# Kernel optimization log

Hardware: AMD Instinct MI355X
Metric: run time of the kernel (lower is better)

## Reference

```python
import jax, jax.numpy as jnp
import numpy as np
from jax import lax

B, T, C, K = 16, 1024, 512, 5
PAD = (K - 1) // 2
EPS_LN = 1e-5
EPS_BN = 1e-5


def setup_inputs() -> dict:
    key = jax.random.key(0)
    ks = jax.random.split(key, 8)
    s1 = 1.0 / np.sqrt(C)          # fan-in of pointwise conv1 (C -> 2C)
    s2 = 1.0 / np.sqrt(2 * C * K)  # fan-in of k=5 conv (2C -> 2C)
    s3 = 1.0 / np.sqrt(C)          # fan-in of pointwise conv3 (C -> C)
    return {
        "x": jax.random.normal(ks[0], (B, T, C), jnp.float32),
        "ln_g": jnp.ones((C,), jnp.float32),
        "ln_b": jnp.zeros((C,), jnp.float32),
        "w1": (jax.random.normal(ks[1], (2 * C, C), jnp.float32) * s1),
        "b1": jnp.zeros((2 * C,), jnp.float32),
        "w2": (jax.random.normal(ks[2], (K, 2 * C, 2 * C), jnp.float32) * s2),  # WIO layout
        "b2": jnp.zeros((2 * C,), jnp.float32),
        "bn_g": jnp.ones((C,), jnp.float32),
        "bn_b": jnp.zeros((C,), jnp.float32),
        "bn_mean": jax.random.normal(ks[3], (C,), jnp.float32) * 0.1,
        "bn_var": jax.random.uniform(ks[4], (C,), jnp.float32, 0.5, 1.5),
        "w3": (jax.random.normal(ks[5], (C, C), jnp.float32) * s3),
        "b3": jnp.zeros((C,), jnp.float32),
    }


def reference(x, ln_g, ln_b, w1, b1, w2, b2, bn_g, bn_b, bn_mean, bn_var, w3, b3):
    # LayerNorm over channel dim (B, T, C)
    mu = jnp.mean(x, axis=-1, keepdims=True)
    var = jnp.mean(jnp.square(x - mu), axis=-1, keepdims=True)
    h = (x - mu) * lax.rsqrt(var + EPS_LN) * ln_g + ln_b

    # pointwise conv C -> 2C (kernel 1 == GEMM), then Swish
    h = jnp.einsum('btc,oc->bto', h, w1) + b1        # (B, T, 2C)
    h = h * jax.nn.sigmoid(h)

    # kernel-5 conv 2C -> 2C, 'same' padding, channels-last
    h = lax.conv_general_dilated(
        h, w2, window_strides=(1,), padding=[(PAD, PAD)],
        dimension_numbers=('NWC', 'WIO', 'NWC')) + b2  # (B, T, 2C)

    # GLU over channel dim: first half * sigmoid(second half)
    a, g = h[..., :C], h[..., C:]
    h = a * jax.nn.sigmoid(g)                        # (B, T, C)

    # BatchNorm1d(C), eval mode (running stats)
    h = (h - bn_mean) * lax.rsqrt(bn_var + EPS_BN) * bn_g + bn_b

    # pointwise conv C -> C; dropout is identity at inference.
    # Torch output is sequential(...)(B,C,T).transpose(1,2) -> (B, T, C)
    return jnp.einsum('btc,oc->bto', h, w3) + b3
```

## Files before the change

kernel.cpp:

```cpp
#include <hip/hip_runtime.h>
#include <cstdint>


#define NB    16
#define TT    1024
#define CC    512
#define C2    1024
#define TPAD  1028

typedef unsigned short u16;
typedef short bf16x8 __attribute__((ext_vector_type(8)));
typedef float f32x4  __attribute__((ext_vector_type(4)));
typedef __attribute__((address_space(3))) u16 lds_u16;
typedef const __attribute__((address_space(1))) u16 glb_u16;

__device__ __forceinline__ float bf2f(u16 u) {
  union { unsigned int i; float f; } v; v.i = ((unsigned int)u) << 16; return v.f;
}
__device__ __forceinline__ u16 f2bf(float f) {
  union { float f; unsigned int i; } v; v.f = f;
  unsigned int x = v.i;
  return (u16)((x + 0x7fffu + ((x >> 16) & 1u)) >> 16);
}

__global__ __launch_bounds__(256) void preproc_k(
    const float* __restrict__ w1, u16* __restrict__ w1b,
    const float* __restrict__ w3, u16* __restrict__ w3b,
    u16* __restrict__ h1p,
    const float* __restrict__ w2, u16* __restrict__ w2t,
    const float* __restrict__ x, const float* __restrict__ lng,
    const float* __restrict__ lnb, u16* __restrict__ hln) {
  __shared__ u16 t[64][65];
  const int b   = blockIdx.x;
  const int tid = threadIdx.x;
  if (b < 512) {
    const int i = (b * 256 + tid) * 4;
    float4 v = *(const float4*)(w1 + i);
    u16 o[4] = { f2bf(v.x), f2bf(v.y), f2bf(v.z), f2bf(v.w) };
    *(uint2*)(w1b + i) = *(const uint2*)o;
  } else if (b < 768) {
    const int i = ((b - 512) * 256 + tid) * 4;
    float4 v = *(const float4*)(w3 + i);
    u16 o[4] = { f2bf(v.x), f2bf(v.y), f2bf(v.z), f2bf(v.w) };
    *(uint2*)(w3b + i) = *(const uint2*)o;
  } else if (b < 800) {
    const int idx = (b - 768) * 256 + tid;
    const int bb  = idx >> 9;
    const int rem = idx & 511;
    const int ri  = rem >> 7;
    const int c8  = (rem & 127) * 8;
    const int row = bb * TPAD + (ri < 2 ? ri : 1024 + ri);
    uint4 z = make_uint4(0u, 0u, 0u, 0u);
    *(uint4*)(h1p + (size_t)row * C2 + c8) = z;
  } else if (b < 2080) {
    const int bt = b - 800;
    const int k  = bt >> 8;
    const int rem = bt & 255;
    const int i0 = (rem & 15) * 64, o0 = (rem >> 4) * 64;
    const int tx = tid & 63, ty = tid >> 6;
    for (int r = ty; r < 64; r += 4)
      t[r][tx] = f2bf(w2[((size_t)(k * C2) + i0 + r) * C2 + o0 + tx]);
    __syncthreads();
    for (int r = ty; r < 64; r += 4)
      w2t[((size_t)(k * C2) + o0 + r) * C2 + i0 + tx] = t[tx][r];
  } else {
    const int tok  = (b - 2080) * 4 + (tid >> 6);
    const int lane = tid & 63;
    const float* xp = x + (size_t)tok * CC + lane * 8;
    float f[8];
    *(float4*)(f)     = *(const float4*)(xp);
    *(float4*)(f + 4) = *(const float4*)(xp + 4);
    float s = 0.f, s2 = 0.f;
#pragma unroll
    for (int j = 0; j < 8; j++) { s += f[j]; s2 += f[j] * f[j]; }
#pragma unroll
    for (int m = 32; m >= 1; m >>= 1) { s += __shfl_xor(s, m, 64); s2 += __shfl_xor(s2, m, 64); }
    const float mu  = s  * (1.f / 512.f);
    const float var = s2 * (1.f / 512.f) - mu * mu;
    const float rs  = rsqrtf(var + 1e-5f);
    u16 ov[8];
#pragma unroll
    for (int j = 0; j < 8; j++) {
      const int c = lane * 8 + j;
      ov[j] = f2bf((f[j] - mu) * rs * lng[c] + lnb[c]);
    }
    *(uint4*)(hln + (size_t)tok * CC + lane * 8) = *(const uint4*)ov;
  }
}

__global__ __launch_bounds__(256, 2) void gemm0_silu(
    const u16* __restrict__ hln, const u16* __restrict__ w1b,
    const float* __restrict__ b1, u16* __restrict__ h1p) {
  __shared__ __align__(16) u16 smem[18432];
  const int tid = threadIdx.x;
  const int mt  = blockIdx.x;
  const int n0  = blockIdx.y * 128;
  const int m0  = mt * 256;
  const int bb  = mt >> 2;
  const int t0  = (mt & 3) * 256;
  const int wave = tid >> 6, lane = tid & 63;
  const int wm = (wave & 1) * 128, wn = (wave >> 1) * 64;
  const int quad = lane >> 4, l16 = lane & 15;
  const int row = tid >> 2;
  const int kc  = (tid & 3) * 8;
  u16* lsB = smem + 8192;

  const u16* Ap0 = hln + (size_t)(m0 + row) * CC + kc;
  const u16* Ap1 = Ap0 + (size_t)64 * CC;
  const u16* Ap2 = Ap0 + (size_t)128 * CC;
  const u16* Ap3 = Ap0 + (size_t)192 * CC;

  const u16* Bb0 = w1b + (size_t)(n0 + wave * 16 + (lane & 15)) * CC + (lane >> 4) * 8;
  const u16* Bb1 = Bb0 + (size_t)64 * CC;

  u16* slA = smem + (tid & 3) * 2048;
  const u16* rdA = smem + quad * 2048;

  f32x4 acc[8][4] = {};
  uint4 rA0, rA1, rA2, rA3;

#define BG0(PTR, GQ, I0)                                                       \
  __builtin_amdgcn_global_load_lds(                                            \
      (glb_u16*)((PTR) + (I0)),                                                \
      (lds_u16*)(lsB + (GQ) * 512), 16, 0, 0);

  rA0 = *(const uint4*)Ap0; rA1 = *(const uint4*)Ap1;
  rA2 = *(const uint4*)Ap2; rA3 = *(const uint4*)Ap3;

#pragma unroll 1
  for (int j = 0; j < 16; j++) {
    __syncthreads();
    {
      const int jb = j * 32;
      BG0(Bb0, wave, jb)
      BG0(Bb1, wave + 4, jb)
    }
    *(uint4*)(slA + row * 8)         = rA0;
    *(uint4*)(slA + (64 + row) * 8)  = rA1;
    *(uint4*)(slA + (128 + row) * 8) = rA2;
    *(uint4*)(slA + (192 + row) * 8) = rA3;
    __syncthreads();
    {
      const int ia = (j + 1 < 16) ? (j + 1) * 32 : 0;
      rA0 = *(const uint4*)(Ap0 + ia);
      rA1 = *(const uint4*)(Ap1 + ia);
      rA2 = *(const uint4*)(Ap2 + ia);
      rA3 = *(const uint4*)(Ap3 + ia);
    }
    bf16x8 bfr[4];
#pragma unroll
    for (int i = 0; i < 4; i++)
      bfr[i] = *(const bf16x8*)(lsB + ((wn >> 4) + i) * 512 + lane * 8);
#pragma unroll
    for (int h = 0; h < 2; h++) {
      bf16x8 af[4];
#pragma unroll
      for (int i = 0; i < 4; i++)
        af[i] = *(const bf16x8*)(rdA + (wm + (h * 4 + i) * 16 + l16) * 8);
#pragma unroll
      for (int mi = 0; mi < 4; mi++)
#pragma unroll
        for (int ni = 0; ni < 4; ni++)
          acc[h * 4 + mi][ni] = __builtin_amdgcn_mfma_f32_16x16x32_bf16(
              af[mi], bfr[ni], acc[h * 4 + mi][ni], 0, 0, 0);
    }
  }
#undef BG0
  __syncthreads();

  float bv[4];
#pragma unroll
  for (int ni = 0; ni < 4; ni++) bv[ni] = b1[n0 + wn + ni * 16 + l16];

  u16* epi = smem + wave * 4608;
#pragma unroll
  for (int h = 0; h < 2; h++) {
#pragma unroll
    for (int mi = 0; mi < 4; mi++)
#pragma unroll
      for (int ni = 0; ni < 4; ni++)
#pragma unroll
        for (int r = 0; r < 4; r++) {
          float v = acc[h * 4 + mi][ni][r] + bv[ni];
          v = v / (1.f + __expf(-v));
          epi[(mi * 16 + quad * 4 + r) * 72 + ni * 16 + l16] = f2bf(v);
        }
#pragma unroll
    for (int p = 0; p < 8; p++) {
      const int rrow = p * 8 + (lane >> 3);
      const int colb = (lane & 7) * 8;
      uint4 v = *(const uint4*)(epi + rrow * 72 + colb);
      const int tt = t0 + wm + h * 64 + rrow;
      *(uint4*)(h1p + (size_t)(bb * TPAD + tt + 2) * C2 + n0 + wn + colb) = v;
    }
  }
}

template <int EPI>
__global__ __launch_bounds__(256, 3) void gemm_bt(
    const u16* __restrict__ A, const u16* __restrict__ Bt,
    const float* __restrict__ bias, void* __restrict__ outv,
    const int Kd, const int ldA) {
  __shared__ __align__(16) u16 smem[20480];
  const int tid  = threadIdx.x;
  const int m0   = blockIdx.x * 128;
  const int n0   = blockIdx.y * 128;
  const int wave = tid >> 6, lane = tid & 63;
  const int wm = (wave & 1) * 64, wn = (wave >> 1) * 64;
  const int quad = lane >> 4, l16 = lane & 15;
  const int row = tid >> 2;
  const int kc  = (tid & 3) * 8;
  const int J = Kd >> 5;

  const u16* Ap0 = A + (size_t)(m0 + row) * ldA + kc;
  const u16* Ap1 = Ap0 + (size_t)64 * ldA;
  const u16* Bp0 = Bt + (size_t)(n0 + row) * Kd + kc;
  const u16* Bp1 = Bp0 + (size_t)64 * Kd;

  f32x4 acc[4][4] = {};
  uint4 rA0 = *(const uint4*)Ap0, rA1 = *(const uint4*)Ap1;
  uint4 rB0 = *(const uint4*)Bp0, rB1 = *(const uint4*)Bp1;
  *(uint4*)(smem + row * 40 + kc)                = rA0;
  *(uint4*)(smem + (64 + row) * 40 + kc)         = rA1;
  *(uint4*)(smem + 10240 + row * 40 + kc)        = rB0;
  *(uint4*)(smem + 10240 + (64 + row) * 40 + kc) = rB1;
  rA0 = *(const uint4*)(Ap0 + 32); rA1 = *(const uint4*)(Ap1 + 32);
  rB0 = *(const uint4*)(Bp0 + 32); rB1 = *(const uint4*)(Bp1 + 32);
  __syncthreads();

#pragma unroll 1
  for (int j = 0; j < J; j++) {
    const u16* curA = smem + (j & 1) * 5120;
    const u16* curB = smem + 10240 + (j & 1) * 5120;
    if (j + 1 < J) {
      u16* nxtA = smem + ((j + 1) & 1) * 5120;
      u16* nxtB = smem + 10240 + ((j + 1) & 1) * 5120;
      *(uint4*)(nxtA + row * 40 + kc)        = rA0;
      *(uint4*)(nxtA + (64 + row) * 40 + kc) = rA1;
      *(uint4*)(nxtB + row * 40 + kc)        = rB0;
      *(uint4*)(nxtB + (64 + row) * 40 + kc) = rB1;
    }
    {
      const int k2 = (j + 2 < J) ? (j + 2) * 32 : 0;
      rA0 = *(const uint4*)(Ap0 + k2); rA1 = *(const uint4*)(Ap1 + k2);
      rB0 = *(const uint4*)(Bp0 + k2); rB1 = *(const uint4*)(Bp1 + k2);
    }
    bf16x8 af[4], bfr[4];
#pragma unroll
    for (int i = 0; i < 4; i++)
      af[i] = *(const bf16x8*)(curA + (wm + i * 16 + l16) * 40 + quad * 8);
#pragma unroll
    for (int i = 0; i < 4; i++)
      bfr[i] = *(const bf16x8*)(curB + (wn + i * 16 + l16) * 40 + quad * 8);
#pragma unroll
    for (int mi = 0; mi < 4; mi++)
#pragma unroll
      for (int ni = 0; ni < 4; ni++)
        acc[mi][ni] = __builtin_amdgcn_mfma_f32_16x16x32_bf16(
            af[mi], bfr[ni], acc[mi][ni], 0, 0, 0);
    __syncthreads();
  }

  float bv[4];
#pragma unroll
  for (int ni = 0; ni < 4; ni++) bv[ni] = bias[n0 + wn + ni * 16 + l16];

  if (EPI == 0) {
    u16* epi = smem + wave * 4608;
#pragma unroll
    for (int mi = 0; mi < 4; mi++)
#pragma unroll
      for (int ni = 0; ni < 4; ni++)
#pragma unroll
        for (int r = 0; r < 4; r++) {
          float v = acc[mi][ni][r] + bv[ni];
          v = v / (1.f + __expf(-v));
          epi[(mi * 16 + quad * 4 + r) * 72 + ni * 16 + l16] = f2bf(v);
        }
    u16* h1p = (u16*)outv;
#pragma unroll
    for (int p = 0; p < 8; p++) {
      const int rrow = p * 8 + (lane >> 3);
      const int colb = (lane & 7) * 8;
      uint4 v = *(const uint4*)(epi + rrow * 72 + colb);
      const int rr = m0 + wm + rrow;
      const int bb = rr >> 10, tt = rr & 1023;
      *(uint4*)(h1p + (size_t)(bb * TPAD + tt + 2) * C2 + n0 + wn + colb) = v;
    }
  } else {
    float* fepi = (float*)(smem + wave * 4608);
    float* outf = (float*)outv;
#pragma unroll
    for (int mi = 0; mi < 4; mi++) {
      float* fp = fepi + (mi & 1) * 1088;
#pragma unroll
      for (int ni = 0; ni < 4; ni++)
#pragma unroll
        for (int r = 0; r < 4; r++)
          fp[(quad * 4 + r) * 68 + ni * 16 + l16] = acc[mi][ni][r] + bv[ni];
#pragma unroll
      for (int p = 0; p < 4; p++) {
        const int rrow = p * 4 + (lane >> 4);
        const int col  = (lane & 15) * 4;
        float4 v = *(const float4*)(fp + rrow * 68 + col);
        *(float4*)(outf + (size_t)(m0 + wm + mi * 16 + rrow) * CC + n0 + wn + col) = v;
      }
    }
  }
}

__global__ __launch_bounds__(256, 2) void conv5_mfma(
    const u16* __restrict__ h1p, const u16* __restrict__ w2t,
    const float* __restrict__ b2,
    const float* __restrict__ bng, const float* __restrict__ bnb,
    const float* __restrict__ bnm, const float* __restrict__ bnv,
    u16* __restrict__ h2) {
  __shared__ __align__(16) u16 smem[28800];
  const int tid = threadIdx.x;
  const int mt  = blockIdx.x;
  const int ya  = blockIdx.y * 64;
  const int bb  = mt >> 2;
  const int t0  = (mt & 3) * 256;
  const size_t arow0 = (size_t)bb * TPAD + t0;
  const int wave = tid >> 6, lane = tid & 63;
  const int wm = (wave & 1) * 128, wn = (wave >> 1) * 64;
  const int quad = lane >> 4, l16 = lane & 15;
  const int row = tid >> 2;
  const int kc  = (tid & 3) * 8;
  u16* lsB = smem + 8320;

  const u16* Ap0 = h1p + (arow0 + row) * C2 + kc;
  const u16* Ap1 = Ap0 + (size_t)64 * C2;
  const u16* Ap2 = Ap0 + (size_t)128 * C2;
  const u16* Ap3 = Ap0 + (size_t)192 * C2;
  const u16* Ap4 = h1p + (arow0 + 256 + row) * C2 + kc;

  const u16* Bb0 = w2t + (size_t)(ya + wave * 16 + (lane & 15)) * C2 + (lane >> 4) * 8;
  const u16* Bb1 = w2t + (size_t)(512 + ya + wave * 16 + (lane & 15)) * C2 + (lane >> 4) * 8;

  u16* slA = smem + (tid & 3) * 2080;
  const u16* rdA = smem + quad * 2080;

  f32x4 acc[8][4] = {};
  uint4 rA0, rA1, rA2, rA3, rA4;

#define BG(PTR, T5, GQ, I0)                                                    \
  __builtin_amdgcn_global_load_lds(                                            \
      (glb_u16*)((PTR) + (size_t)(T5) * C2 * C2 + (I0)),                       \
      (lds_u16*)(lsB + ((T5) * 8 + (GQ)) * 512), 16, 0, 0);

  rA0 = *(const uint4*)Ap0; rA1 = *(const uint4*)Ap1;
  rA2 = *(const uint4*)Ap2; rA3 = *(const uint4*)Ap3;
  if (tid < 16) rA4 = *(const uint4*)Ap4;

#pragma unroll 1
  for (int j = 0; j < 32; j++) {
    __syncthreads();
    {
      const int ib0 = j * 32;
#pragma unroll
      for (int t5 = 0; t5 < 5; t5++) {
        BG(Bb0, t5, wave, ib0)
        BG(Bb1, t5, wave + 4, ib0)
      }
    }
    *(uint4*)(slA + row * 8)         = rA0;
    *(uint4*)(slA + (64 + row) * 8)  = rA1;
    *(uint4*)(slA + (128 + row) * 8) = rA2;
    *(uint4*)(slA + (192 + row) * 8) = rA3;
    if (tid < 16) *(uint4*)(slA + (256 + row) * 8) = rA4;
    __syncthreads();
    {
      const int ia = (j + 1 < 32) ? (j + 1) * 32 : 0;
      rA0 = *(const uint4*)(Ap0 + ia);
      rA1 = *(const uint4*)(Ap1 + ia);
      rA2 = *(const uint4*)(Ap2 + ia);
      rA3 = *(const uint4*)(Ap3 + ia);
      if (tid < 16) rA4 = *(const uint4*)(Ap4 + ia);
    }
#pragma unroll
    for (int k = 0; k < 5; k++) {
      bf16x8 bfr[4];
#pragma unroll
      for (int i = 0; i < 4; i++)
        bfr[i] = *(const bf16x8*)(lsB + (k * 8 + (wn >> 4) + i) * 512 + lane * 8);
#pragma unroll
      for (int h = 0; h < 2; h++) {
        bf16x8 af[4];
#pragma unroll
        for (int i = 0; i < 4; i++)
          af[i] = *(const bf16x8*)(rdA + (wm + (h * 4 + i) * 16 + l16 + k) * 8);
#pragma unroll
        for (int mi = 0; mi < 4; mi++)
#pragma unroll
          for (int ni = 0; ni < 4; ni++)
            acc[h * 4 + mi][ni] = __builtin_amdgcn_mfma_f32_16x16x32_bf16(
                af[mi], bfr[ni], acc[h * 4 + mi][ni], 0, 0, 0);
      }
    }
  }
#undef BG
  __syncthreads();

  float bv[4];
#pragma unroll
  for (int ni = 0; ni < 4; ni++)
    bv[ni] = b2[(wn >> 6) * 512 + ya + ni * 16 + l16];

  const int cb8 = (lane & 7) * 8;
  float sc8[8], bm8[8], bb8[8];
#pragma unroll
  for (int jj = 0; jj < 8; jj++) {
    const int c = ya + cb8 + jj;
    sc8[jj] = bng[c] * rsqrtf(bnv[c] + 1e-5f);
    bm8[jj] = bnm[c];
    bb8[jj] = bnb[c];
  }

  u16* abuf = smem;
  u16* gbuf = smem + 9216;
  const size_t orow0 = (size_t)bb * TT + t0;
#pragma unroll 1
  for (int hh = 0; hh < 2; hh++) {
    if ((wave & 1) == hh) {
      u16* buf = (wn >> 6) ? gbuf : abuf;
#pragma unroll
      for (int mi = 0; mi < 8; mi++)
#pragma unroll
        for (int ni = 0; ni < 4; ni++)
#pragma unroll
          for (int r = 0; r < 4; r++)
            buf[(mi * 16 + quad * 4 + r) * 72 + ni * 16 + l16] =
                f2bf(acc[mi][ni][r] + bv[ni]);
    }
    __syncthreads();
#pragma unroll
    for (int p = 0; p < 4; p++) {
      const int rr = wave * 32 + p * 8 + (lane >> 3);
      uint4 va = *(const uint4*)(abuf + rr * 72 + cb8);
      uint4 vg = *(const uint4*)(gbuf + rr * 72 + cb8);
      u16 aa[8], gg[8], oo[8];
      *(uint4*)aa = va; *(uint4*)gg = vg;
#pragma unroll
      for (int jj = 0; jj < 8; jj++) {
        const float a = bf2f(aa[jj]);
        const float g = bf2f(gg[jj]);
        const float h = a / (1.f + __expf(-g));
        oo[jj] = f2bf((h - bm8[jj]) * sc8[jj] + bb8[jj]);
      }
      *(uint4*)(h2 + (orow0 + hh * 128 + rr) * CC + ya + cb8) = *(const uint4*)oo;
    }
    __syncthreads();
  }
}

extern "C" void kernel_launch(void* const* d_in, const int* in_sizes, int n_in,
                              void* d_out, int out_size, void* d_ws, size_t ws_size,
                              hipStream_t stream) {
  const float* x   = (const float*)d_in[0];
  const float* lng = (const float*)d_in[1];
  const float* lnb = (const float*)d_in[2];
  const float* w1  = (const float*)d_in[3];
  const float* b1  = (const float*)d_in[4];
  const float* w2  = (const float*)d_in[5];
  const float* b2  = (const float*)d_in[6];
  const float* bng = (const float*)d_in[7];
  const float* bnb = (const float*)d_in[8];
  const float* bnm = (const float*)d_in[9];
  const float* bnv = (const float*)d_in[10];
  const float* w3  = (const float*)d_in[11];
  const float* b3  = (const float*)d_in[12];

  u16* ws  = (u16*)d_ws;
  u16* hln = ws;
  u16* h2  = hln;
  u16* h1p = ws + 8388608;
  u16* w2t = h1p + 16842752;
  u16* hcv = w2t + 5242880;
  u16* w1b = hcv + 16777216;
  u16* w3b = w1b + 524288;

  preproc_k  <<<6176, 256, 0, stream>>>(w1, w1b, w3, w3b, h1p, w2, w2t,
                                        x, lng, lnb, hln);
  gemm0_silu <<<dim3(64, 8), 256, 0, stream>>>(hln, w1b, b1, h1p);
  conv5_mfma <<<dim3(64, 8), 256, 0, stream>>>(h1p, w2t, b2, bng, bnb, bnm, bnv, h2);
  gemm_bt<1> <<<dim3(128, 4), 256, 0, stream>>>(h2, w3b, b3, d_out, 512, 512);
}
```

Measured before the change: 312.4 us.

## Switch conv5 GEMM from 16x16x32 to 32x32x16 bf16 MFMA tiles

Replaces the 16x16x32 MFMA inner loop of the k=5 conv kernel with 32x32x16 MFMAs. Each wave now owns a 128x64 output tile as 4x2 32x32 accumulators, with the B-operand LDS layout and A-fragment reads reorganised to match. The epilogue scatter is rewritten for the 32x32 accumulator lane and row mapping. The aim is fewer LDS fragment reads per FLOP and fewer MFMA issues; the cost is different LDS bank-access patterns and register usage under the 2-wave occupancy bound.

```diff
diff --git a/kernel.cpp b/kernel.cpp
--- a/kernel.cpp
+++ b/kernel.cpp
@@ -11,6 +11,7 @@
 typedef unsigned short u16;
 typedef short bf16x8 __attribute__((ext_vector_type(8)));
 typedef float f32x4  __attribute__((ext_vector_type(4)));
+typedef float f32x16 __attribute__((ext_vector_type(16)));
 typedef __attribute__((address_space(3))) u16 lds_u16;
 typedef const __attribute__((address_space(1))) u16 glb_u16;
 
@@ -323,8 +324,8 @@
   const int t0  = (mt & 3) * 256;
   const size_t arow0 = (size_t)bb * TPAD + t0;
   const int wave = tid >> 6, lane = tid & 63;
-  const int wm = (wave & 1) * 128, wn = (wave >> 1) * 64;
-  const int quad = lane >> 4, l16 = lane & 15;
+  const int wm  = (wave & 1) * 128;
+  const int l32 = lane & 31, lh = lane >> 5;
   const int row = tid >> 2;
   const int kc  = (tid & 3) * 8;
   u16* lsB = smem + 8320;
@@ -335,19 +336,19 @@
   const u16* Ap3 = Ap0 + (size_t)192 * C2;
   const u16* Ap4 = h1p + (arow0 + 256 + row) * C2 + kc;
 
-  const u16* Bb0 = w2t + (size_t)(ya + wave * 16 + (lane & 15)) * C2 + (lane >> 4) * 8;
-  const u16* Bb1 = w2t + (size_t)(512 + ya + wave * 16 + (lane & 15)) * C2 + (lane >> 4) * 8;
+  const int gcb = (wave < 2) ? (ya + wave * 32) : (512 + ya + (wave - 2) * 32);
+  const u16* Bq0 = w2t + (size_t)(gcb + l32) * C2 + lh * 8;
+  const u16* Bq1 = Bq0 + 16;
 
   u16* slA = smem + (tid & 3) * 2080;
-  const u16* rdA = smem + quad * 2080;
-
-  f32x4 acc[8][4] = {};
+
+  f32x16 acc[4][2] = {};
   uint4 rA0, rA1, rA2, rA3, rA4;
 
-#define BG(PTR, T5, GQ, I0)                                                    \
+#define BG32(T5, Q, PTR, I0)                                                   \
   __builtin_amdgcn_global_load_lds(                                            \
       (glb_u16*)((PTR) + (size_t)(T5) * C2 * C2 + (I0)),                       \
-      (lds_u16*)(lsB + ((T5) * 8 + (GQ)) * 512), 16, 0, 0);
+      (lds_u16*)(lsB + ((T5) * 4 + wave) * 1024 + (Q) * 512), 16, 0, 0);
 
   rA0 = *(const uint4*)Ap0; rA1 = *(const uint4*)Ap1;
   rA2 = *(const uint4*)Ap2; rA3 = *(const uint4*)Ap3;
@@ -360,8 +361,8 @@
       const int ib0 = j * 32;
 #pragma unroll
       for (int t5 = 0; t5 < 5; t5++) {
-        BG(Bb0, t5, wave, ib0)
-        BG(Bb1, t5, wave + 4, ib0)
+        BG32(t5, 0, Bq0, ib0)
+        BG32(t5, 1, Bq1, ib0)
       }
     }
     *(uint4*)(slA + row * 8)         = rA0;
@@ -380,32 +381,34 @@
     }
 #pragma unroll
     for (int k = 0; k < 5; k++) {
-      bf16x8 bfr[4];
-#pragma unroll
-      for (int i = 0; i < 4; i++)
-        bfr[i] = *(const bf16x8*)(lsB + (k * 8 + (wn >> 4) + i) * 512 + lane * 8);
-#pragma unroll
-      for (int h = 0; h < 2; h++) {
+#pragma unroll
+      for (int kh = 0; kh < 2; kh++) {
+        const int oct = kh * 2 + lh;
+        bf16x8 bfr0 = *(const bf16x8*)(
+            lsB + (k * 4 + (wave >> 1) * 2 + 0) * 1024 + oct * 256 + l32 * 8);
+        bf16x8 bfr1 = *(const bf16x8*)(
+            lsB + (k * 4 + (wave >> 1) * 2 + 1) * 1024 + oct * 256 + l32 * 8);
         bf16x8 af[4];
 #pragma unroll
-        for (int i = 0; i < 4; i++)
-          af[i] = *(const bf16x8*)(rdA + (wm + (h * 4 + i) * 16 + l16 + k) * 8);
-#pragma unroll
         for (int mi = 0; mi < 4; mi++)
-#pragma unroll
-          for (int ni = 0; ni < 4; ni++)
-            acc[h * 4 + mi][ni] = __builtin_amdgcn_mfma_f32_16x16x32_bf16(
-                af[mi], bfr[ni], acc[h * 4 + mi][ni], 0, 0, 0);
+          af[mi] = *(const bf16x8*)(
+              smem + oct * 2080 + (wm + mi * 32 + l32 + k) * 8);
+#pragma unroll
+        for (int mi = 0; mi < 4; mi++) {
+          acc[mi][0] = __builtin_amdgcn_mfma_f32_32x32x16_bf16(
+              af[mi], bfr0, acc[mi][0], 0, 0, 0);
+          acc[mi][1] = __builtin_amdgcn_mfma_f32_32x32x16_bf16(
+              af[mi], bfr1, acc[mi][1], 0, 0, 0);
+        }
       }
     }
   }
-#undef BG
+#undef BG32
   __syncthreads();
 
-  float bv[4];
-#pragma unroll
-  for (int ni = 0; ni < 4; ni++)
-    bv[ni] = b2[(wn >> 6) * 512 + ya + ni * 16 + l16];
+  const int cb = (wave >> 1) ? (512 + ya) : ya;
+  const float bv0 = b2[cb + l32];
+  const float bv1 = b2[cb + 32 + l32];
 
   const int cb8 = (lane & 7) * 8;
   float sc8[8], bm8[8], bb8[8];
@@ -423,15 +426,17 @@
 #pragma unroll 1
   for (int hh = 0; hh < 2; hh++) {
     if ((wave & 1) == hh) {
-      u16* buf = (wn >> 6) ? gbuf : abuf;
-#pragma unroll
-      for (int mi = 0; mi < 8; mi++)
-#pragma unroll
-        for (int ni = 0; ni < 4; ni++)
-#pragma unroll
-          for (int r = 0; r < 4; r++)
-            buf[(mi * 16 + quad * 4 + r) * 72 + ni * 16 + l16] =
-                f2bf(acc[mi][ni][r] + bv[ni]);
+      u16* buf = (wave >> 1) ? gbuf : abuf;
+#pragma unroll
+      for (int mi = 0; mi < 4; mi++)
+#pragma unroll
+        for (int ni = 0; ni < 2; ni++)
+#pragma unroll
+          for (int r = 0; r < 16; r++) {
+            const int rr = mi * 32 + (r & 3) + 8 * (r >> 2) + 4 * lh;
+            buf[rr * 72 + ni * 32 + l32] =
+                f2bf(acc[mi][ni][r] + (ni ? bv1 : bv0));
+          }
     }
     __syncthreads();
 #pragma unroll
```

Measured after the change: 323.7 us. 1.04x slower.
